# Performance work log

Hardware: AMD Instinct MI355X
Metric: run time of the kernel (lower is better)

Reference implementation:

```python
import jax, jax.numpy as jnp
import numpy as np

FEATURE_DIM = 128
EDGE_DIM = 32
N_NODES = 10000
BATCH = 4
N_EDGES = 640000
TEMPERATURE = 0.66
POWER_ITERS = 5


def spectral_normalize(W):
    # torch.nn.utils.spectral_norm: divide W by largest singular value estimated
    # via power iteration; u, v are treated as constants (no grad).
    # W: [out, in]
    u = jnp.ones((W.shape[0],), W.dtype) / jnp.sqrt(jnp.asarray(W.shape[0], W.dtype))
    for _ in range(POWER_ITERS):
        v = W.T @ u
        v = v / (jnp.linalg.norm(v) + 1e-12)
        u = W @ v
        u = u / (jnp.linalg.norm(u) + 1e-12)
    u = jax.lax.stop_gradient(u)
    v = jax.lax.stop_gradient(v)
    sigma = u @ (W @ v)
    return W / sigma


def setup_inputs() -> dict:
    key = jax.random.key(0)
    ks = jax.random.split(key, 8)
    node_feat = jax.random.normal(ks[0], (BATCH, N_NODES, FEATURE_DIM), dtype=jnp.float32)
    batch_ids = jax.random.randint(ks[1], (N_EDGES,), 0, BATCH)
    src_nodes = jax.random.randint(ks[2], (N_EDGES,), 0, N_NODES)
    tgt_nodes = jax.random.randint(ks[3], (N_EDGES,), 0, N_NODES)
    in_dim = 2 * FEATURE_DIM + 1  # src_feat ++ tgt_feat ++ distance
    # kaiming_normal_(nonlinearity='relu'): std = sqrt(2 / fan_in)
    W1 = jax.random.normal(ks[4], (EDGE_DIM, in_dim), jnp.float32) * np.sqrt(2.0 / in_dim)
    b1 = jnp.zeros((EDGE_DIM,), jnp.float32)
    W2 = jax.random.normal(ks[5], (EDGE_DIM, EDGE_DIM), jnp.float32) * np.sqrt(2.0 / EDGE_DIM)
    b2 = jnp.zeros((EDGE_DIM,), jnp.float32)
    bound = 0.1 * np.sqrt(6.0 / (EDGE_DIM + 1))
    W3 = jax.random.uniform(ks[6], (1, EDGE_DIM), jnp.float32, -bound, bound)
    b3 = jnp.ones((1,), jnp.float32)
    return {"node_feat": node_feat, "W1": W1, "b1": b1, "W2": W2, "b2": b2,
            "W3": W3, "b3": b3, "batch_ids": batch_ids,
            "src_nodes": src_nodes, "tgt_nodes": tgt_nodes}


def reference(node_feat, W1, b1, W2, b2, W3, b3, batch_ids, src_nodes, tgt_nodes):
    # per-edge gather of endpoint features  [E, D]
    src_feat = node_feat[batch_ids, src_nodes]
    tgt_feat = node_feat[batch_ids, tgt_nodes]
    dist = jnp.linalg.norm(src_feat - tgt_feat, axis=-1, keepdims=True)  # [E,1]
    edge_features = jnp.concatenate([src_feat, tgt_feat, dist], axis=-1)  # [E, 2D+1]
    # spectral-norm MLP (dropout is identity at eval / in this reference)
    h = jax.nn.relu(edge_features @ spectral_normalize(W1).T + b1)
    h = jax.nn.relu(h @ spectral_normalize(W2).T + b2)
    logAlpha = (h @ spectral_normalize(W3).T + b3).squeeze(-1)  # [E]
    logAlpha = jnp.clip(logAlpha, -5.0, 5.0)
    edge_weights = jax.nn.sigmoid(logAlpha / TEMPERATURE)
    return edge_weights, logAlpha
```

## Files before the change

### kernel.cpp

```cpp
#include <hip/hip_runtime.h>
#include <hip/hip_fp16.h>
#include <math.h>

#define FEATD 128
#define NNODES 10000
#define NBATCH 4
#define NROWS (NBATCH*NNODES)

#define OFF_I1   0
#define OFF_W1L  8
#define OFF_W2   64
#define OFF_W3   1088
#define OFF_W2H  1120
#define OFF_P16  4096
#define P16_FLOATS (NROWS*64/2)
#define OFF_FQ   (OFF_P16 + P16_FLOATS)
#define F16_FLOATS (NROWS*FEATD/2)
#define OFF_FBWT OFF_P16

#define WSTRIDE 68

typedef _Float16 h2 __attribute__((ext_vector_type(2)));
union U32H2 { unsigned u; h2 h; };
union U4H2  { uint4 u; h2 h[4]; };

#if defined(__has_builtin)
#if __has_builtin(__builtin_amdgcn_fdot2)
#define HAVE_FDOT2 1
#endif
#if __has_builtin(__builtin_amdgcn_cvt_pk_f32_fp8) && __has_builtin(__builtin_amdgcn_cvt_pk_fp8_f32)
#define HAVE_FP8 1
#endif
#endif

__device__ __forceinline__ float fdot2f(h2 a, h2 b, float c) {
#ifdef HAVE_FDOT2
  return __builtin_amdgcn_fdot2(a, b, c, false);
#else
  return c + (float)a[0] * (float)b[0] + (float)a[1] * (float)b[1];
#endif
}

#ifdef HAVE_FP8
typedef float floatx2 __attribute__((ext_vector_type(2)));
__device__ __forceinline__ float ssd_fp8_w(unsigned aw, unsigned bw, float s) {
  floatx2 al = __builtin_amdgcn_cvt_pk_f32_fp8((int)aw, false);
  floatx2 ah = __builtin_amdgcn_cvt_pk_f32_fp8((int)aw, true);
  floatx2 bl = __builtin_amdgcn_cvt_pk_f32_fp8((int)bw, false);
  floatx2 bh = __builtin_amdgcn_cvt_pk_f32_fp8((int)bw, true);
  float d0 = al[0] - bl[0], d1 = al[1] - bl[1];
  float d2 = ah[0] - bh[0], d3 = ah[1] - bh[1];
  return s + d0 * d0 + d1 * d1 + d2 * d2 + d3 * d3;
}
__device__ __forceinline__ float grp_dist_fp8(uint2 au, uint2 bu) {
  float ssd = ssd_fp8_w(au.x, bu.x, 0.f);
  ssd = ssd_fp8_w(au.y, bu.y, ssd);
  ssd += __shfl_xor(ssd, 1, 64);
  ssd += __shfl_xor(ssd, 2, 64);
  ssd += __shfl_xor(ssd, 4, 64);
  ssd += __shfl_xor(ssd, 8, 64);
  return sqrtf(ssd);
}
#endif

template <int M, int K>
__device__ float spectral_sigma_t(const float* __restrict__ Wg,
                                  float* sW, float* u, float* v, volatile float* red) {
  int tid = threadIdx.x;
  int wid = tid >> 6, lid = tid & 63;
  int j8 = tid >> 3, l8 = tid & 7;
  for (int i = tid; i < M * K; i += 256) sW[i] = Wg[i];
  if (tid < M) u[tid] = 1.0f;
  __syncthreads();
  float invu = 1.0f / sqrtf((float)M);
  float invv = 0.f;

  for (int it = 0; it < 5; ++it) {
    float p = 0.f;
    for (int k = tid; k < K; k += 256) {
      float a = 0.f;
      #pragma unroll
      for (int j = 0; j < M; ++j) a += sW[j * K + k] * u[j];
      a *= invu;
      v[k] = a;
      p += a * a;
    }
    #pragma unroll
    for (int off = 1; off < 64; off <<= 1) p += __shfl_xor(p, off, 64);
    if (lid == 0) red[wid] = p;
    __syncthreads();
    p = red[0] + red[1] + red[2] + red[3];
    invv = 1.0f / (sqrtf(p) + 1e-12f);

    float a = 0.f;
    if (j8 < M) {
      #pragma unroll
      for (int k = l8; k < K; k += 8) a += sW[j8 * K + k] * v[k];
      a *= invv;
    }
    a += __shfl_xor(a, 1, 64);
    a += __shfl_xor(a, 2, 64);
    a += __shfl_xor(a, 4, 64);
    float q = 0.f;
    if (j8 < M && l8 == 0) { u[j8] = a; q = a * a; }
    #pragma unroll
    for (int off = 1; off < 64; off <<= 1) q += __shfl_xor(q, off, 64);
    if (lid == 0) red[4 + wid] = q;
    __syncthreads();
    q = red[4] + red[5] + red[6] + red[7];
    invu = 1.0f / (sqrtf(q) + 1e-12f);
  }

  float a = 0.f;
  if (j8 < M) {
    #pragma unroll
    for (int k = l8; k < K; k += 8) a += sW[j8 * K + k] * v[k];
  }
  a += __shfl_xor(a, 1, 64);
  a += __shfl_xor(a, 2, 64);
  a += __shfl_xor(a, 4, 64);
  float s = (j8 < M && l8 == 0) ? a * u[j8] : 0.f;
  #pragma unroll
  for (int off = 1; off < 64; off <<= 1) s += __shfl_xor(s, off, 64);
  if (lid == 0) red[wid] = s;
  __syncthreads();
  float sig = (red[0] + red[1] + red[2] + red[3]) * invu * invv;
  __syncthreads();
  return sig;
}

__global__ __launch_bounds__(256, 4) void prep_kernel(const float* __restrict__ feat,
                                                      const float* __restrict__ W1,
                                                      const float* __restrict__ W2,
                                                      const float* __restrict__ W3,
                                                      float* __restrict__ ws,
                                                      int doFQ) {
  __shared__ float sA[128 * WSTRIDE];
  __shared__ float u[32], v[257];
  __shared__ float red[8];
  int tid = threadIdx.x;

  if (blockIdx.x == 0) {
    float sig1 = spectral_sigma_t<32, 257>(W1, sA, u, v, red);
    float i1 = 1.0f / sig1;
    if (tid == 0) ws[OFF_I1] = i1;
    for (int j = tid; j < 32; j += 256) ws[OFF_W1L + j] = sA[j * 257 + 256] * i1;
    __syncthreads();
    float sig2 = spectral_sigma_t<32, 32>(W2, sA, u, v, red);
    float i2 = 1.0f / sig2;
    for (int idx = tid; idx < 1024; idx += 256) ws[OFF_W2 + idx] = sA[idx] * i2;
    unsigned* w2h = (unsigned*)(ws + OFF_W2H);
    for (int idx = tid; idx < 512; idx += 256) {
      int j = idx >> 4, q = idx & 15;
      U32H2 pk;
      pk.h[0] = (_Float16)(sA[j * 32 + 2 * q] * i2);
      pk.h[1] = (_Float16)(sA[j * 32 + 2 * q + 1] * i2);
      w2h[idx] = pk.u;
    }
    __syncthreads();
    float sig3 = spectral_sigma_t<1, 32>(W3, sA, u, v, red);
    float i3 = 1.0f / sig3;
    for (int k = tid; k < 32; k += 256) ws[OFF_W3 + k] = sA[k] * i3;
    return;
  }

  for (int idx = tid; idx < 32 * 257; idx += 256) {
    int j = idx / 257, c = idx - j * 257;
    float w = W1[idx];
    if (c < 128) sA[c * WSTRIDE + j] = w;
    else if (c < 256) sA[(c - 128) * WSTRIDE + 32 + j] = w;
  }
  __syncthreads();

  __half* p16 = (__half*)(ws + OFF_P16);
  char* fq = (char*)(ws + OFF_FQ);
  int rg = tid >> 4;
  int jg = (tid & 15) << 2;
  int slice = tid & 15;
  int r0 = (blockIdx.x - 1) * 64 + rg * 4;
  const float4* F0 = (const float4*)&feat[(size_t)(r0 + 0) * FEATD];
  const float4* F1 = (const float4*)&feat[(size_t)(r0 + 1) * FEATD];
  const float4* F2 = (const float4*)&feat[(size_t)(r0 + 2) * FEATD];
  const float4* F3 = (const float4*)&feat[(size_t)(r0 + 3) * FEATD];
  float acc[4][4] = {{0,0,0,0},{0,0,0,0},{0,0,0,0},{0,0,0,0}};

  #pragma unroll 2
  for (int k4 = 0; k4 < 32; ++k4) {
    float4 f0 = F0[k4], f1 = F1[k4], f2 = F2[k4], f3 = F3[k4];
    if (doFQ && (k4 >> 1) == slice) {
#ifdef HAVE_FP8
      unsigned w;
      w = __builtin_amdgcn_cvt_pk_fp8_f32(f0.x, f0.y, 0, false);
      w = __builtin_amdgcn_cvt_pk_fp8_f32(f0.z, f0.w, (int)w, true);
      *(unsigned*)(fq + (size_t)(r0 + 0) * 128 + (size_t)k4 * 4) = w;
      w = __builtin_amdgcn_cvt_pk_fp8_f32(f1.x, f1.y, 0, false);
      w = __builtin_amdgcn_cvt_pk_fp8_f32(f1.z, f1.w, (int)w, true);
      *(unsigned*)(fq + (size_t)(r0 + 1) * 128 + (size_t)k4 * 4) = w;
      w = __builtin_amdgcn_cvt_pk_fp8_f32(f2.x, f2.y, 0, false);
      w = __builtin_amdgcn_cvt_pk_fp8_f32(f2.z, f2.w, (int)w, true);
      *(unsigned*)(fq + (size_t)(r0 + 2) * 128 + (size_t)k4 * 4) = w;
      w = __builtin_amdgcn_cvt_pk_fp8_f32(f3.x, f3.y, 0, false);
      w = __builtin_amdgcn_cvt_pk_fp8_f32(f3.z, f3.w, (int)w, true);
      *(unsigned*)(fq + (size_t)(r0 + 3) * 128 + (size_t)k4 * 4) = w;
#else
      U32H2 a, b; uint2 pk;
      a.h[0]=(_Float16)f0.x; a.h[1]=(_Float16)f0.y; b.h[0]=(_Float16)f0.z; b.h[1]=(_Float16)f0.w;
      pk.x=a.u; pk.y=b.u; *(uint2*)(fq + (size_t)(r0+0)*256 + (size_t)k4*8) = pk;
      a.h[0]=(_Float16)f1.x; a.h[1]=(_Float16)f1.y; b.h[0]=(_Float16)f1.z; b.h[1]=(_Float16)f1.w;
      pk.x=a.u; pk.y=b.u; *(uint2*)(fq + (size_t)(r0+1)*256 + (size_t)k4*8) = pk;
      a.h[0]=(_Float16)f2.x; a.h[1]=(_Float16)f2.y; b.h[0]=(_Float16)f2.z; b.h[1]=(_Float16)f2.w;
      pk.x=a.u; pk.y=b.u; *(uint2*)(fq + (size_t)(r0+2)*256 + (size_t)k4*8) = pk;
      a.h[0]=(_Float16)f3.x; a.h[1]=(_Float16)f3.y; b.h[0]=(_Float16)f3.z; b.h[1]=(_Float16)f3.w;
      pk.x=a.u; pk.y=b.u; *(uint2*)(fq + (size_t)(r0+3)*256 + (size_t)k4*8) = pk;
#endif
    }
    #pragma unroll
    for (int kk = 0; kk < 4; ++kk) {
      int k = 4 * k4 + kk;
      float4 w = *(const float4*)&sA[k * WSTRIDE + jg];
      float e0 = (kk == 0) ? f0.x : (kk == 1) ? f0.y : (kk == 2) ? f0.z : f0.w;
      float e1 = (kk == 0) ? f1.x : (kk == 1) ? f1.y : (kk == 2) ? f1.z : f1.w;
      float e2 = (kk == 0) ? f2.x : (kk == 1) ? f2.y : (kk == 2) ? f2.z : f2.w;
      float e3 = (kk == 0) ? f3.x : (kk == 1) ? f3.y : (kk == 2) ? f3.z : f3.w;
      acc[0][0] += e0 * w.x; acc[0][1] += e0 * w.y; acc[0][2] += e0 * w.z; acc[0][3] += e0 * w.w;
      acc[1][0] += e1 * w.x; acc[1][1] += e1 * w.y; acc[1][2] += e1 * w.z; acc[1][3] += e1 * w.w;
      acc[2][0] += e2 * w.x; acc[2][1] += e2 * w.y; acc[2][2] += e2 * w.z; acc[2][3] += e2 * w.w;
      acc[3][0] += e3 * w.x; acc[3][1] += e3 * w.y; acc[3][2] += e3 * w.z; acc[3][3] += e3 * w.w;
    }
  }
  #pragma unroll
  for (int r = 0; r < 4; ++r) {
    U32H2 a, b;
    a.h[0] = (_Float16)acc[r][0]; a.h[1] = (_Float16)acc[r][1];
    b.h[0] = (_Float16)acc[r][2]; b.h[1] = (_Float16)acc[r][3];
    uint2 o; o.x = a.u; o.y = b.u;
    *(uint2*)((char*)p16 + (size_t)(r0 + r) * 128 + (size_t)jg * 2) = o;
  }
}

__device__ __forceinline__ float grp_dist_f16(uint4 au, uint4 bu) {
  U4H2 a, b; a.u = au; b.u = bu;
  float ssd = 0.f;
  #pragma unroll
  for (int p = 0; p < 4; ++p) { h2 d = a.h[p] - b.h[p]; ssd = fdot2f(d, d, ssd); }
  ssd += __shfl_xor(ssd, 1, 64);
  ssd += __shfl_xor(ssd, 2, 64);
  ssd += __shfl_xor(ssd, 4, 64);
  ssd += __shfl_xor(ssd, 8, 64);
  return sqrtf(ssd);
}

__device__ __forceinline__ unsigned h1pack(unsigned puv, unsigned quv, float dist, float i1,
                                           float w1l0, float w1l1, float bb0, float bb1) {
  U32H2 p, q; p.u = puv; q.u = quv;
  float h0  = fmaxf(fmaf((float)p.h[0] + (float)q.h[0], i1, fmaf(dist, w1l0, bb0)), 0.f);
  float h1v = fmaxf(fmaf((float)p.h[1] + (float)q.h[1], i1, fmaf(dist, w1l1, bb1)), 0.f);
  U32H2 r; r.h[0] = (_Float16)h0; r.h[1] = (_Float16)h1v;
  return r.u;
}

template <bool FQ>
__global__ __launch_bounds__(256, 8) void edge_fused(const float* __restrict__ feat,
                                                     const float* __restrict__ ws,
                                                     const float* __restrict__ b1,
                                                     const float* __restrict__ b2,
                                                     const float* __restrict__ b3,
                                                     const int* __restrict__ bids,
                                                     const int* __restrict__ srcs,
                                                     const int* __restrict__ tgts,
                                                     float* __restrict__ out, int E) {
  __shared__ unsigned ht[256 * 17];
  __shared__ int sRS[256], sRT[256];
  int tid = threadIdx.x;
  int lane = tid & 15;
  int grp  = tid >> 4;

  const char*  featq = (const char*)(ws + OFF_FQ);
  const __half* p16  = (const __half*)(ws + OFF_P16);
  const unsigned* w2h = (const unsigned*)(ws + OFF_W2H);

  float i1 = ws[OFF_I1];
  int j0 = 2 * lane;
  float w1l0 = ws[OFF_W1L + j0];
  float w1l1 = ws[OFF_W1L + j0 + 1];
  float bb0  = b1[j0];
  float bb1  = b1[j0 + 1];
  float bias3 = b3[0];

  for (int base = blockIdx.x * 256; base < E; base += gridDim.x * 256) {
    int e0 = base + tid;
    if (e0 < E) {
      int b = bids[e0];
      sRS[tid] = b * NNODES + srcs[e0];
      sRT[tid] = b * NNODES + tgts[e0];
    }
    __syncthreads();

    if (FQ && (base + 256 <= E)) {
      #pragma unroll 1
      for (int rr = 0; rr < 8; ++rr) {
        int el0 = (rr * 2 + 0) * 16 + grp;
        int el1 = (rr * 2 + 1) * 16 + grp;
        int rs0 = sRS[el0], rt0 = sRT[el0];
        int rs1 = sRS[el1], rt1 = sRT[el1];
#ifdef HAVE_FP8
        uint2 a0 = *(const uint2*)(featq + ((size_t)rs0 << 7) + (lane << 3));
        uint2 c0 = *(const uint2*)(featq + ((size_t)rt0 << 7) + (lane << 3));
        uint2 a1 = *(const uint2*)(featq + ((size_t)rs1 << 7) + (lane << 3));
        uint2 c1 = *(const uint2*)(featq + ((size_t)rt1 << 7) + (lane << 3));
#else
        uint4 a0 = *(const uint4*)(featq + ((size_t)rs0 << 8) + (lane << 4));
        uint4 c0 = *(const uint4*)(featq + ((size_t)rt0 << 8) + (lane << 4));
        uint4 a1 = *(const uint4*)(featq + ((size_t)rs1 << 8) + (lane << 4));
        uint4 c1 = *(const uint4*)(featq + ((size_t)rt1 << 8) + (lane << 4));
#endif
        unsigned pu0 = *(const unsigned*)((const char*)p16 + ((size_t)rs0 << 7) + (lane << 2));
        unsigned qu0 = *(const unsigned*)((const char*)p16 + ((size_t)rt0 << 7) + 64 + (lane << 2));
        unsigned pu1 = *(const unsigned*)((const char*)p16 + ((size_t)rs1 << 7) + (lane << 2));
        unsigned qu1 = *(const unsigned*)((const char*)p16 + ((size_t)rt1 << 7) + 64 + (lane << 2));
#ifdef HAVE_FP8
        float d0 = grp_dist_fp8(a0, c0);
        float d1 = grp_dist_fp8(a1, c1);
#else
        float d0 = grp_dist_f16(a0, c0);
        float d1 = grp_dist_f16(a1, c1);
#endif
        ht[el0 * 17 + lane] = h1pack(pu0, qu0, d0, i1, w1l0, w1l1, bb0, bb1);
        ht[el1 * 17 + lane] = h1pack(pu1, qu1, d1, i1, w1l0, w1l1, bb0, bb1);
      }
    } else {
      #pragma unroll 2
      for (int rr = 0; rr < 16; ++rr) {
        int el = rr * 16 + grp;
        int e  = base + el;
        if (e < E) {
          int rs = sRS[el], rt = sRT[el];
          float dist;
          if (FQ) {
#ifdef HAVE_FP8
            uint2 au = *(const uint2*)(featq + ((size_t)rs << 7) + (lane << 3));
            uint2 bu = *(const uint2*)(featq + ((size_t)rt << 7) + (lane << 3));
            dist = grp_dist_fp8(au, bu);
#else
            uint4 au = *(const uint4*)(featq + ((size_t)rs << 8) + (lane << 4));
            uint4 bu = *(const uint4*)(featq + ((size_t)rt << 8) + (lane << 4));
            dist = grp_dist_f16(au, bu);
#endif
          } else {
            const float4* A  = (const float4*)&feat[(size_t)rs * FEATD];
            const float4* Bp = (const float4*)&feat[(size_t)rt * FEATD];
            float ssd = 0.f;
            #pragma unroll
            for (int p = 0; p < 2; ++p) {
              float4 a = A[lane * 2 + p], c = Bp[lane * 2 + p];
              float dx = a.x - c.x, dy = a.y - c.y, dz = a.z - c.z, dw = a.w - c.w;
              ssd += dx * dx + dy * dy + dz * dz + dw * dw;
            }
            ssd += __shfl_xor(ssd, 1, 64);
            ssd += __shfl_xor(ssd, 2, 64);
            ssd += __shfl_xor(ssd, 4, 64);
            ssd += __shfl_xor(ssd, 8, 64);
            dist = sqrtf(ssd);
          }
          unsigned puv = *(const unsigned*)((const char*)p16 + ((size_t)rs << 7) + (lane << 2));
          unsigned quv = *(const unsigned*)((const char*)p16 + ((size_t)rt << 7) + 64 + (lane << 2));
          ht[el * 17 + lane] = h1pack(puv, quv, dist, i1, w1l0, w1l1, bb0, bb1);
        }
      }
    }
    __syncthreads();

    int e = base + tid;
    if (e < E) {
      unsigned hrow[16];
      #pragma unroll
      for (int q = 0; q < 16; ++q) hrow[q] = ht[tid * 17 + q];
      float la = bias3;
      #pragma unroll
      for (int j = 0; j < 32; ++j) {
        float acc = b2[j];
        #pragma unroll
        for (int q = 0; q < 16; ++q) {
          U32H2 w; w.u = w2h[j * 16 + q];
          U32H2 h; h.u = hrow[q];
          acc = fdot2f(w.h, h.h, acc);
        }
        la += ws[OFF_W3 + j] * fmaxf(acc, 0.f);
      }
      la = fminf(fmaxf(la, -5.f), 5.f);
      out[e]     = 1.0f / (1.0f + exp2f(la * -2.18590179f));
      out[E + e] = la;
    }
    __syncthreads();
  }
}

__global__ __launch_bounds__(256) void spectral_full(const float* __restrict__ W1,
                                                     const float* __restrict__ W2,
                                                     const float* __restrict__ W3,
                                                     float* __restrict__ ws) {
  __shared__ float sA[32 * 257];
  __shared__ float u[32], v[257];
  __shared__ float red[8];
  int tid = threadIdx.x;
  float sig1 = spectral_sigma_t<32, 257>(W1, sA, u, v, red);
  float i1 = 1.0f / sig1;
  for (int idx = tid; idx < 128 * 64; idx += 256) {
    int k = idx >> 6, jj = idx & 63;
    float w = (jj < 32) ? sA[jj * 257 + k] : sA[(jj - 32) * 257 + 128 + k];
    ws[OFF_FBWT + idx] = w * i1;
  }
  for (int j = tid; j < 32; j += 256) ws[OFF_W1L + j] = sA[j * 257 + 256] * i1;
  __syncthreads();
  float sig2 = spectral_sigma_t<32, 32>(W2, sA, u, v, red);
  float i2 = 1.0f / sig2;
  for (int idx = tid; idx < 1024; idx += 256) ws[OFF_W2 + idx] = sA[idx] * i2;
  __syncthreads();
  float sig3 = spectral_sigma_t<1, 32>(W3, sA, u, v, red);
  float i3 = 1.0f / sig3;
  for (int k = tid; k < 32; k += 256) ws[OFF_W3 + k] = sA[k] * i3;
}

__global__ __launch_bounds__(256) void edge_kernel_nop(const float* __restrict__ feat,
                                                       const float* __restrict__ ws,
                                                       const float* __restrict__ b1,
                                                       const float* __restrict__ b2,
                                                       const float* __restrict__ b3,
                                                       const int* __restrict__ bids,
                                                       const int* __restrict__ srcs,
                                                       const int* __restrict__ tgts,
                                                       float* __restrict__ out, int E) {
  __shared__ float sWt[128 * 64];
  __shared__ float sW2[1024];
  __shared__ float sW3[32], sW1l[32], sB1[32], sB2[32];
  int tid = threadIdx.x;
  for (int i = tid * 4; i < 128 * 64; i += 256 * 4)
    *(float4*)&sWt[i] = *(const float4*)&ws[OFF_FBWT + i];
  for (int i = tid; i < 1024; i += 256) sW2[i] = ws[OFF_W2 + i];
  if (tid < 32) {
    sW3[tid]  = ws[OFF_W3 + tid];
    sW1l[tid] = ws[OFF_W1L + tid];
    sB1[tid]  = b1[tid];
    sB2[tid]  = b2[tid];
  }
  __syncthreads();
  float bias3 = b3[0];

  for (int e = blockIdx.x * 256 + tid; e < E; e += gridDim.x * 256) {
    int b = bids[e], s = srcs[e], t = tgts[e];
    const float4* A  = (const float4*)&feat[(size_t)(b * NNODES + s) * FEATD];
    const float4* Bp = (const float4*)&feat[(size_t)(b * NNODES + t) * FEATD];
    float ssd = 0.f;
    float h1p[32];
    #pragma unroll
    for (int j = 0; j < 32; ++j) h1p[j] = 0.f;
    #pragma unroll 1
    for (int k4 = 0; k4 < 32; ++k4) {
      float4 a = A[k4], c = Bp[k4];
      float dx = a.x - c.x, dy = a.y - c.y, dz = a.z - c.z, dw = a.w - c.w;
      ssd += dx * dx + dy * dy + dz * dz + dw * dw;
      #pragma unroll
      for (int kk = 0; kk < 4; ++kk) {
        int k = 4 * k4 + kk;
        float fa = (kk == 0) ? a.x : (kk == 1) ? a.y : (kk == 2) ? a.z : a.w;
        float fc = (kk == 0) ? c.x : (kk == 1) ? c.y : (kk == 2) ? c.z : c.w;
        #pragma unroll
        for (int q = 0; q < 8; ++q) {
          float4 w0 = *(const float4*)&sWt[k * 64 + 4 * q];
          float4 w1 = *(const float4*)&sWt[k * 64 + 32 + 4 * q];
          h1p[4*q+0] += fa * w0.x + fc * w1.x;
          h1p[4*q+1] += fa * w0.y + fc * w1.y;
          h1p[4*q+2] += fa * w0.z + fc * w1.z;
          h1p[4*q+3] += fa * w0.w + fc * w1.w;
        }
      }
    }
    float dist = sqrtf(ssd);
    float h1[32];
    #pragma unroll
    for (int j = 0; j < 32; ++j)
      h1[j] = fmaxf(h1p[j] + dist * sW1l[j] + sB1[j], 0.f);
    float la = bias3;
    #pragma unroll
    for (int j = 0; j < 32; ++j) {
      float acc = sB2[j];
      #pragma unroll
      for (int q = 0; q < 8; ++q) {
        float4 w = *(const float4*)&sW2[j * 32 + 4 * q];
        acc += w.x * h1[4 * q] + w.y * h1[4 * q + 1] + w.z * h1[4 * q + 2] + w.w * h1[4 * q + 3];
      }
      la += sW3[j] * fmaxf(acc, 0.f);
    }
    la = fminf(fmaxf(la, -5.f), 5.f);
    out[e]     = 1.0f / (1.0f + __expf(-la / 0.66f));
    out[E + e] = la;
  }
}

extern "C" void kernel_launch(void* const* d_in, const int* in_sizes, int n_in,
                              void* d_out, int out_size, void* d_ws, size_t ws_size,
                              hipStream_t stream) {
  const float* feat = (const float*)d_in[0];
  const float* W1   = (const float*)d_in[1];
  const float* b1   = (const float*)d_in[2];
  const float* W2   = (const float*)d_in[3];
  const float* b2   = (const float*)d_in[4];
  const float* W3   = (const float*)d_in[5];
  const float* b3   = (const float*)d_in[6];
  const int* bids   = (const int*)d_in[7];
  const int* srcs   = (const int*)d_in[8];
  const int* tgts   = (const int*)d_in[9];
  float* out = (float*)d_out;
  float* ws  = (float*)d_ws;
  int E = in_sizes[7];

  size_t need_p  = (size_t)OFF_FQ * sizeof(float);
  size_t need_fq = (size_t)(OFF_FQ + F16_FLOATS) * sizeof(float);
  int egrid = (E + 255) / 256;

  if (ws_size >= need_fq) {
    prep_kernel<<<dim3(626), dim3(256), 0, stream>>>(feat, W1, W2, W3, ws, 1);
    edge_fused<true><<<dim3(egrid), dim3(256), 0, stream>>>(feat, ws, b1, b2, b3,
                                                            bids, srcs, tgts, out, E);
  } else if (ws_size >= need_p) {
    prep_kernel<<<dim3(626), dim3(256), 0, stream>>>(feat, W1, W2, W3, ws, 0);
    edge_fused<false><<<dim3(egrid), dim3(256), 0, stream>>>(feat, ws, b1, b2, b3,
                                                             bids, srcs, tgts, out, E);
  } else {
    spectral_full<<<dim3(1), dim3(256), 0, stream>>>(W1, W2, W3, ws);
    edge_kernel_nop<<<dim3(egrid), dim3(256), 0, stream>>>(feat, ws, b1, b2, b3,
                                                           bids, srcs, tgts, out, E);
  }
}
```

Measured before the change: 92.80 us.

## Make edge kernel wave-local: shuffle indices, per-wave LDS tile, drop block barriers

Restructures the fused edge kernel so each 64-lane wave owns 64 edges. Edge indices are passed between lanes with shuffles instead of shared memory, and each wave uses a private LDS slice of the hidden tile. This removes all __syncthreads barriers and lets waves proceed independently. The gather loop also goes from two to four edges per iteration for more memory-level parallelism, at the cost of more live registers. Correctness depends on wave size being 64, with no barrier between the wave's own LDS writes and reads.

```diff
diff --git a/kernel.cpp b/kernel.cpp
--- a/kernel.cpp
+++ b/kernel.cpp
@@ -260,20 +260,22 @@
 }
 
 template <bool FQ>
-__global__ __launch_bounds__(256, 8) void edge_fused(const float* __restrict__ feat,
-                                                     const float* __restrict__ ws,
-                                                     const float* __restrict__ b1,
-                                                     const float* __restrict__ b2,
-                                                     const float* __restrict__ b3,
-                                                     const int* __restrict__ bids,
-                                                     const int* __restrict__ srcs,
-                                                     const int* __restrict__ tgts,
-                                                     float* __restrict__ out, int E) {
-  __shared__ unsigned ht[256 * 17];
-  __shared__ int sRS[256], sRT[256];
+__global__ __launch_bounds__(256, 8) void edge_wave(const float* __restrict__ feat,
+                                                    const float* __restrict__ ws,
+                                                    const float* __restrict__ b1,
+                                                    const float* __restrict__ b2,
+                                                    const float* __restrict__ b3,
+                                                    const int* __restrict__ bids,
+                                                    const int* __restrict__ srcs,
+                                                    const int* __restrict__ tgts,
+                                                    float* __restrict__ out, int E) {
+  __shared__ unsigned ht[4 * 64 * 17];
   int tid = threadIdx.x;
-  int lane = tid & 15;
-  int grp  = tid >> 4;
+  int wv   = tid >> 6;
+  int l64  = tid & 63;
+  int grp  = l64 >> 4;
+  int lane = l64 & 15;
+  unsigned* htw = &ht[wv * 64 * 17];
 
   const char*  featq = (const char*)(ws + OFF_FQ);
   const __half* p16  = (const __half*)(ws + OFF_P16);
@@ -287,54 +289,78 @@
   float bb1  = b1[j0 + 1];
   float bias3 = b3[0];
 
-  for (int base = blockIdx.x * 256; base < E; base += gridDim.x * 256) {
-    int e0 = base + tid;
-    if (e0 < E) {
-      int b = bids[e0];
-      sRS[tid] = b * NNODES + srcs[e0];
-      sRT[tid] = b * NNODES + tgts[e0];
-    }
-    __syncthreads();
-
-    if (FQ && (base + 256 <= E)) {
+  int wstep = gridDim.x * 4 * 64;
+  for (int base = (blockIdx.x * 4 + wv) * 64; base < E; base += wstep) {
+    int e = base + l64;
+    int rs_m = 0, rt_m = 0;
+    if (e < E) {
+      int b = bids[e];
+      rs_m = b * NNODES + srcs[e];
+      rt_m = b * NNODES + tgts[e];
+    }
+
+    if (FQ && (base + 64 <= E)) {
+      int elb = grp << 4;
       #pragma unroll 1
-      for (int rr = 0; rr < 8; ++rr) {
-        int el0 = (rr * 2 + 0) * 16 + grp;
-        int el1 = (rr * 2 + 1) * 16 + grp;
-        int rs0 = sRS[el0], rt0 = sRT[el0];
-        int rs1 = sRS[el1], rt1 = sRT[el1];
+      for (int rr = 0; rr < 4; ++rr) {
+        int el0 = elb + 4 * rr + 0;
+        int el1 = elb + 4 * rr + 1;
+        int el2 = elb + 4 * rr + 2;
+        int el3 = elb + 4 * rr + 3;
+        int rs0 = __shfl(rs_m, el0, 64), rt0 = __shfl(rt_m, el0, 64);
+        int rs1 = __shfl(rs_m, el1, 64), rt1 = __shfl(rt_m, el1, 64);
+        int rs2 = __shfl(rs_m, el2, 64), rt2 = __shfl(rt_m, el2, 64);
+        int rs3 = __shfl(rs_m, el3, 64), rt3 = __shfl(rt_m, el3, 64);
 #ifdef HAVE_FP8
         uint2 a0 = *(const uint2*)(featq + ((size_t)rs0 << 7) + (lane << 3));
         uint2 c0 = *(const uint2*)(featq + ((size_t)rt0 << 7) + (lane << 3));
         uint2 a1 = *(const uint2*)(featq + ((size_t)rs1 << 7) + (lane << 3));
         uint2 c1 = *(const uint2*)(featq + ((size_t)rt1 << 7) + (lane << 3));
+        uint2 a2 = *(const uint2*)(featq + ((size_t)rs2 << 7) + (lane << 3));
+        uint2 c2 = *(const uint2*)(featq + ((size_t)rt2 << 7) + (lane << 3));
+        uint2 a3 = *(const uint2*)(featq + ((size_t)rs3 << 7) + (lane << 3));
+        uint2 c3 = *(const uint2*)(featq + ((size_t)rt3 << 7) + (lane << 3));
 #else
         uint4 a0 = *(const uint4*)(featq + ((size_t)rs0 << 8) + (lane << 4));
         uint4 c0 = *(const uint4*)(featq + ((size_t)rt0 << 8) + (lane << 4));
         uint4 a1 = *(const uint4*)(featq + ((size_t)rs1 << 8) + (lane << 4));
         uint4 c1 = *(const uint4*)(featq + ((size_t)rt1 << 8) + (lane << 4));
+        uint4 a2 = *(const uint4*)(featq + ((size_t)rs2 << 8) + (lane << 4));
+        uint4 c2 = *(const uint4*)(featq + ((size_t)rt2 << 8) + (lane << 4));
+        uint4 a3 = *(const uint4*)(featq + ((size_t)rs3 << 8) + (lane << 4));
+        uint4 c3 = *(const uint4*)(featq + ((size_t)rt3 << 8) + (lane << 4));
 #endif
         unsigned pu0 = *(const unsigned*)((const char*)p16 + ((size_t)rs0 << 7) + (lane << 2));
         unsigned qu0 = *(const unsigned*)((const char*)p16 + ((size_t)rt0 << 7) + 64 + (lane << 2));
         unsigned pu1 = *(const unsigned*)((const char*)p16 + ((size_t)rs1 << 7) + (lane << 2));
         unsigned qu1 = *(const unsigned*)((const char*)p16 + ((size_t)rt1 << 7) + 64 + (lane << 2));
+        unsigned pu2 = *(const unsigned*)((const char*)p16 + ((size_t)rs2 << 7) + (lane << 2));
+        unsigned qu2 = *(const unsigned*)((const char*)p16 + ((size_t)rt2 << 7) + 64 + (lane << 2));
+        unsigned pu3 = *(const unsigned*)((const char*)p16 + ((size_t)rs3 << 7) + (lane << 2));
+        unsigned qu3 = *(const unsigned*)((const char*)p16 + ((size_t)rt3 << 7) + 64 + (lane << 2));
 #ifdef HAVE_FP8
         float d0 = grp_dist_fp8(a0, c0);
         float d1 = grp_dist_fp8(a1, c1);
+        float d2 = grp_dist_fp8(a2, c2);
+        float d3 = grp_dist_fp8(a3, c3);
 #else
         float d0 = grp_dist_f16(a0, c0);
         float d1 = grp_dist_f16(a1, c1);
-#endif
-        ht[el0 * 17 + lane] = h1pack(pu0, qu0, d0, i1, w1l0, w1l1, bb0, bb1);
-        ht[el1 * 17 + lane] = h1pack(pu1, qu1, d1, i1, w1l0, w1l1, bb0, bb1);
+        float d2 = grp_dist_f16(a2, c2);
+        float d3 = grp_dist_f16(a3, c3);
+#endif
+        htw[el0 * 17 + lane] = h1pack(pu0, qu0, d0, i1, w1l0, w1l1, bb0, bb1);
+        htw[el1 * 17 + lane] = h1pack(pu1, qu1, d1, i1, w1l0, w1l1, bb0, bb1);
+        htw[el2 * 17 + lane] = h1pack(pu2, qu2, d2, i1, w1l0, w1l1, bb0, bb1);
+        htw[el3 * 17 + lane] = h1pack(pu3, qu3, d3, i1, w1l0, w1l1, bb0, bb1);
       }
     } else {
+      int elb = grp << 4;
       #pragma unroll 2
-      for (int rr = 0; rr < 16; ++rr) {
-        int el = rr * 16 + grp;
-        int e  = base + el;
-        if (e < E) {
-          int rs = sRS[el], rt = sRT[el];
+      for (int r = 0; r < 16; ++r) {
+        int el = elb + r;
+        if (base + el < E) {
+          int rs = __shfl(rs_m, el, 64), rt = __shfl(rt_m, el, 64);
           float dist;
           if (FQ) {
 #ifdef HAVE_FP8
@@ -364,17 +390,15 @@
           }
           unsigned puv = *(const unsigned*)((const char*)p16 + ((size_t)rs << 7) + (lane << 2));
           unsigned quv = *(const unsigned*)((const char*)p16 + ((size_t)rt << 7) + 64 + (lane << 2));
-          ht[el * 17 + lane] = h1pack(puv, quv, dist, i1, w1l0, w1l1, bb0, bb1);
+          htw[el * 17 + lane] = h1pack(puv, quv, dist, i1, w1l0, w1l1, bb0, bb1);
         }
       }
     }
-    __syncthreads();
-
-    int e = base + tid;
+
     if (e < E) {
       unsigned hrow[16];
       #pragma unroll
-      for (int q = 0; q < 16; ++q) hrow[q] = ht[tid * 17 + q];
+      for (int q = 0; q < 16; ++q) hrow[q] = htw[l64 * 17 + q];
       float la = bias3;
       #pragma unroll
       for (int j = 0; j < 32; ++j) {
@@ -391,7 +415,6 @@
       out[e]     = 1.0f / (1.0f + exp2f(la * -2.18590179f));
       out[E + e] = la;
     }
-    __syncthreads();
   }
 }
 
@@ -520,12 +543,12 @@
 
   if (ws_size >= need_fq) {
     prep_kernel<<<dim3(626), dim3(256), 0, stream>>>(feat, W1, W2, W3, ws, 1);
-    edge_fused<true><<<dim3(egrid), dim3(256), 0, stream>>>(feat, ws, b1, b2, b3,
-                                                            bids, srcs, tgts, out, E);
+    edge_wave<true><<<dim3(egrid), dim3(256), 0, stream>>>(feat, ws, b1, b2, b3,
+                                                           bids, srcs, tgts, out, E);
   } else if (ws_size >= need_p) {
     prep_kernel<<<dim3(626), dim3(256), 0, stream>>>(feat, W1, W2, W3, ws, 0);
-    edge_fused<false><<<dim3(egrid), dim3(256), 0, stream>>>(feat, ws, b1, b2, b3,
-                                                             bids, srcs, tgts, out, E);
+    edge_wave<false><<<dim3(egrid), dim3(256), 0, stream>>>(feat, ws, b1, b2, b3,
+                                                            bids, srcs, tgts, out, E);
   } else {
     spectral_full<<<dim3(1), dim3(256), 0, stream>>>(W1, W2, W3, ws);
     edge_kernel_nop<<<dim3(egrid), dim3(256), 0, stream>>>(feat, ws, b1, b2, b3,
```

New measurement: 91.56 us, median of 2. No clear change (-1.3%).
